# Kernel tuning notes

Measured on AMD Instinct MI355X. Metric: run time of the kernel, lower is better.

The kernel has to match this reference:

```python
import jax, jax.numpy as jnp
import numpy as np

N, IN_DIM, E, H, L, M = 65536, 512, 128, 4, 2, 256
DH = E // H  # 32

def _gaussian_orthogonal(m, d, rng):
    # FAVOR+ gaussian orthogonal random matrix (performer_pytorch, scaling=0)
    blocks = []
    for _ in range((m + d - 1) // d):
        q, _ = np.linalg.qr(rng.normal(size=(d, d)))
        blocks.append(q.T)
    mat = np.concatenate(blocks)[:m]
    mult = np.linalg.norm(rng.normal(size=(m, d)), axis=1)
    return (mult[:, None] * mat).astype(np.float32)

def setup_inputs() -> dict:
    rng = np.random.default_rng(0)
    r = lambda *s: jnp.asarray(rng.normal(size=s, scale=0.02), jnp.float32)
    z = lambda *s: jnp.zeros(s, jnp.float32)
    o = lambda *s: jnp.ones(s, jnp.float32)
    return dict(
        x=jnp.asarray(rng.normal(size=(N, IN_DIM)), dtype=jnp.float32),
        Wpin=r(IN_DIM, E), bpin=z(E),
        lag=o(L, E), lab=z(L, E),                    # performer inner pre-LN (attn)
        Wq=r(L, E, E), Wk=r(L, E, E), Wv=r(L, E, E), # qkv (no bias in performer_pytorch)
        Wo=r(L, E, E), bo=z(L, E),                   # attn to_out
        lbg=o(L, E), lbb=z(L, E),                    # performer inner pre-LN (ff)
        Wf1=r(L, E, 4 * E), bf1=z(L, 4 * E),         # performer inner GELU FFN
        Wf2=r(L, 4 * E, E), bf2=z(L, E),
        Wpo=r(L, E, E), bpo=z(L, E),                 # PerformerSelfAttention.out_proj
        n1g=o(L, E), n1b=z(L, E),                    # block norm1
        Wn1=r(L, E, 4 * E), bn1=z(L, 4 * E),         # block ReLU FFN
        Wn2=r(L, 4 * E, E), bn2=z(L, E),
        n2g=o(L, E), n2b=z(L, E),                    # block norm2
        Wc=r(E, 1), bc=z(1),                         # classifier
        proj=jnp.stack([jnp.asarray(_gaussian_orthogonal(M, DH, rng)) for _ in range(L)]),
    )

def _ln(x, g, b, eps=1e-5):
    mu = x.mean(-1, keepdims=True)
    var = ((x - mu) ** 2).mean(-1, keepdims=True)
    return (x - mu) * jax.lax.rsqrt(var + eps) * g + b

def _softmax_kernel(data, proj, is_query, eps=1e-4):
    # data: [1,H,N,DH]; proj: [M,DH]  (performer_pytorch softmax_kernel)
    dn = data.shape[-1] ** -0.25
    ratio = proj.shape[0] ** -0.5
    dd = jnp.einsum('bhnd,md->bhnm', data * dn, proj)
    diag = (data ** 2).sum(-1, keepdims=True) * 0.5 * (dn * dn)
    stab = jnp.max(dd, -1, keepdims=True) if is_query else jnp.max(dd)
    return ratio * (jnp.exp(dd - diag - stab) + eps)

def _linear_attn(qf, kf, v):
    # non-causal FAVOR+: O(N*M*DH)
    D = jnp.einsum('bhnm,bhm->bhn', qf, kf.sum(-2))          # denominator
    ctx = jnp.einsum('bhnm,bhnd->bhmd', kf, v)               # [1,H,M,DH]
    return jnp.einsum('bhnm,bhmd->bhnd', qf, ctx) / D[..., None]

def _forward(x, Wpin, bpin, lag, lab, Wq, Wk, Wv, Wo, bo, lbg, lbb,
             Wf1, bf1, Wf2, bf2, Wpo, bpo, n1g, n1b, Wn1, bn1, Wn2, bn2,
             n2g, n2b, Wc, bc, proj):
    h = (x @ Wpin + bpin)[None]  # [1,N,E]
    split = lambda t: t.reshape(1, -1, H, DH).transpose(0, 2, 1, 3)
    for l in range(L):
        # --- inner Performer (depth=1): pre-LN attn + pre-LN GELU FFN, residuals ---
        y = _ln(h, lag[l], lab[l])
        q, k, v = split(y @ Wq[l]), split(y @ Wk[l]), split(y @ Wv[l])
        qf = _softmax_kernel(q, proj[l], True)
        kf = _softmax_kernel(k, proj[l], False)
        a = _linear_attn(qf, kf, v).transpose(0, 2, 1, 3).reshape(1, -1, E)
        h1 = h + (a @ Wo[l] + bo[l])
        y2 = _ln(h1, lbg[l], lbb[l])
        h2 = h1 + (jax.nn.gelu(y2 @ Wf1[l] + bf1[l], approximate=False) @ Wf2[l] + bf2[l])
        # --- outer block: post-LN residual attn + post-LN ReLU FFN ---
        attn_out = h2 @ Wpo[l] + bpo[l]
        h = _ln(h + attn_out, n1g[l], n1b[l])
        ffn = jax.nn.relu(h @ Wn1[l] + bn1[l]) @ Wn2[l] + bn2[l]
        h = _ln(h + ffn, n2g[l], n2b[l])
    return jax.nn.sigmoid(h[0] @ Wc + bc)[:, 0]  # [N]

def reference(x, Wpin, bpin, lag, lab, Wq, Wk, Wv, Wo, bo, lbg, lbb,
              Wf1, bf1, Wf2, bf2, Wpo, bpo, n1g, n1b, Wn1, bn1, Wn2, bn2,
              n2g, n2b, Wc, bc, proj):
    return _forward(x, Wpin, bpin, lag, lab, Wq, Wk, Wv, Wo, bo, lbg, lbb,
                    Wf1, bf1, Wf2, bf2, Wpo, bpo, n1g, n1b, Wn1, bn1, Wn2, bn2,
                    n2g, n2b, Wc, bc, proj)
```

## Files before the change

### kernel.cpp

```cpp
#include <hip/hip_runtime.h>
#include <math.h>

#define NTOK  65536
#define EDIM  128
#define HN    4
#define DHD   32
#define MF    256
#define LLAYERS 2
#define INDIM 512
#define FDIM  512
#define CR    512
#define NCHK  (NTOK/CR)

#define DN    0.4204482076268573f
#define DN2   0.17677669529663687f
#define KEPS  1e-4f

typedef unsigned short u16;
typedef unsigned int   u32;
typedef __attribute__((ext_vector_type(8))) __bf16 bf16x8;
typedef __attribute__((ext_vector_type(4))) float  f32x4;

__device__ __forceinline__ u16 f2bf(float f){
  u32 u = __float_as_uint(f);
  u32 r = (u + 0x7fffu + ((u >> 16) & 1u)) >> 16;
  return (u16)r;
}
__device__ __forceinline__ float bf2f(u16 h){ return __uint_as_float(((u32)h) << 16); }

__device__ __forceinline__ void gload_lds16(const void* g, void* l){
  __builtin_amdgcn_global_load_lds(
      (const __attribute__((address_space(1))) u32*)g,
      (__attribute__((address_space(3))) u32*)l, 16, 0, 0);
}

struct PrepArgs {
  const float* Wpin; const float* Wq; const float* Wk; const float* Wv;
  const float* Wo;   const float* Wpo; const float* Wf1; const float* Wf2;
  const float* Wn1;  const float* Wn2; const float* proj;
};

__global__ __launch_bounds__(256) void prep_kernel(PrepArgs a, u16* __restrict__ wts,
                                                   u16* __restrict__ pjb)
{
  int idx = blockIdx.x * 256 + threadIdx.x;
  const float* sp; u16* dp; int r, K, J;
  if      (idx <  65536) { sp = a.Wpin; dp = wts;          r = idx;          K = 512; J = 128; }
  else if (idx <  98304) { sp = a.Wq;   dp = wts +  65536; r = idx -  65536; K = 128; J = 128; }
  else if (idx < 131072) { sp = a.Wk;   dp = wts +  98304; r = idx -  98304; K = 128; J = 128; }
  else if (idx < 163840) { sp = a.Wv;   dp = wts + 131072; r = idx - 131072; K = 128; J = 128; }
  else if (idx < 196608) { sp = a.Wo;   dp = wts + 163840; r = idx - 163840; K = 128; J = 128; }
  else if (idx < 229376) { sp = a.Wpo;  dp = wts + 196608; r = idx - 196608; K = 128; J = 128; }
  else if (idx < 360448) { sp = a.Wf1;  dp = wts + 229376; r = idx - 229376; K = 128; J = 512; }
  else if (idx < 491520) { sp = a.Wf2;  dp = wts + 360448; r = idx - 360448; K = 512; J = 128; }
  else if (idx < 622592) { sp = a.Wn1;  dp = wts + 491520; r = idx - 491520; K = 128; J = 512; }
  else if (idx < 753664) { sp = a.Wn2;  dp = wts + 622592; r = idx - 622592; K = 512; J = 128; }
  else { int p = idx - 753664; pjb[p] = f2bf(a.proj[p] * DN); return; }
  int kj = K * J;
  int l = r / kj, rr = r - l * kj;
  int j = rr / K, k = rr - j * K;
  dp[r] = f2bf(sp[(size_t)l * kj + (size_t)k * J + j]);
}

template<int LNM, bool A32, bool MULTI>
__global__ __launch_bounds__(256, 4) void gemm_f(
    const u16* __restrict__ A, const float* __restrict__ Af,
    const u16* __restrict__ Bt,
    const float* __restrict__ bias, const u16* __restrict__ res,
    u16* __restrict__ outRaw, int K, int J, int op,
    const float* __restrict__ g1, const float* __restrict__ b1, u16* __restrict__ outL1,
    u16* __restrict__ outAux,
    const float* __restrict__ Wcp, const float* __restrict__ bcp, float* __restrict__ outCls)
{
  __shared__ __align__(16) u16 pool[18432];
  __shared__ float lnred[2][2][32][2];
  u16* Al = pool;
  u16* Bl = pool + 6144;
  const int tid  = threadIdx.x;
  const int lane = tid & 63;
  const int w    = tid >> 6;
  const int wr   = w >> 1, wc = w & 1;
  const int bid  = blockIdx.x;
  const int nwg8 = gridDim.x >> 3;
  const int bsw  = (bid & 7) * nwg8 + (bid >> 3);
  const int n0   = bsw * 64;
  const int jb   = MULTI ? 0 : blockIdx.y * 128;
  const u16* Bu  = MULTI ? (Bt + (size_t)blockIdx.y * 32768) : Bt;

  f32x4 acc[2][4];
#pragma unroll
  for (int m = 0; m < 2; ++m)
#pragma unroll
    for (int n = 0; n < 4; ++n) acc[m][n] = (f32x4){0.f, 0.f, 0.f, 0.f};

  const int srow = lane >> 2;
  const int skg  = (lane & 3) ^ ((lane >> 3) & 3);

  auto stageB = [&](int buf, int k0) {
#pragma unroll
    for (int i = 0; i < 2; ++i) {
      const int rb = 2 * w + i;
      gload_lds16(Bu + (size_t)(jb + rb * 16 + srow) * K + k0 + skg * 8,
                  &Bl[buf * 4096 + rb * 512]);
    }
  };
  auto stageA16 = [&](int buf, int k0) {
    gload_lds16(A + (size_t)(n0 + w * 16 + srow) * K + k0 + skg * 8,
                &Al[buf * 2048 + w * 512]);
  };

  const int r16f = lane & 15;
  const int kgl  = (lane >> 4) ^ ((lane >> 1) & 3);
  const int foff = r16f * 32 + kgl * 8;

  auto compute = [&](int cur) {
    bf16x8 af[2], bfg[4];
#pragma unroll
    for (int m = 0; m < 2; ++m)
      af[m]  = *reinterpret_cast<const bf16x8*>(&Al[cur * 2048 + (wr * 2 + m) * 512 + foff]);
#pragma unroll
    for (int n = 0; n < 4; ++n)
      bfg[n] = *reinterpret_cast<const bf16x8*>(&Bl[cur * 4096 + (wc * 4 + n) * 512 + foff]);
#pragma unroll
    for (int m = 0; m < 2; ++m)
#pragma unroll
      for (int n = 0; n < 4; ++n)
        acc[m][n] = __builtin_amdgcn_mfma_f32_16x16x32_bf16(af[m], bfg[n], acc[m][n], 0, 0, 0);
  };

  if constexpr (A32) {
    constexpr int T = 16;
    float4 fA[3][2];
    const int r = tid >> 2, hf = tid & 3;
    auto loadA = [&](int slot, int k0) {
      const float* gp = Af + (size_t)(n0 + r) * 512 + k0 + hf * 8;
      fA[slot][0] = ((const float4*)gp)[0];
      fA[slot][1] = ((const float4*)gp)[1];
    };
    const int rbA = r >> 4, r16A = r & 15, swzA = (r16A >> 1) & 3;
    auto writeA = [&](int slot, int buf) {
      uint4 p0;
      p0.x = (u32)f2bf(fA[slot][0].x) | ((u32)f2bf(fA[slot][0].y) << 16);
      p0.y = (u32)f2bf(fA[slot][0].z) | ((u32)f2bf(fA[slot][0].w) << 16);
      p0.z = (u32)f2bf(fA[slot][1].x) | ((u32)f2bf(fA[slot][1].y) << 16);
      p0.w = (u32)f2bf(fA[slot][1].z) | ((u32)f2bf(fA[slot][1].w) << 16);
      *reinterpret_cast<uint4*>(&Al[buf * 2048 + rbA * 512 + r16A * 32 + (hf ^ swzA) * 8]) = p0;
    };
    loadA(0, 0); loadA(1, 32); loadA(2, 64);
    stageB(0, 0); stageB(1, 32);
    asm volatile("s_waitcnt vmcnt(8)" ::: "memory");
    writeA(0, 0);
#pragma unroll
    for (int t = 0; t < T; ++t) {
      if (t + 2 < T) asm volatile("s_waitcnt vmcnt(4) lgkmcnt(0)" ::: "memory");
      else           asm volatile("s_waitcnt vmcnt(0) lgkmcnt(0)" ::: "memory");
      __builtin_amdgcn_s_barrier();
      if (t + 1 < T) writeA((t + 1) % 3, (t + 1) % 3);
      if (t + 3 < T) loadA((t + 3) % 3, (t + 3) * 32);
      if (t + 2 < T) stageB((t + 2) % 3, (t + 2) * 32);
      compute(t % 3);
    }
    __builtin_amdgcn_s_barrier();
  } else {
    const int T = K >> 5;
    stageA16(0, 0); stageB(0, 0);
    stageA16(1, 32); stageB(1, 32);
    for (int t = 0; t < T; ++t) {
      if (t + 1 < T) asm volatile("s_waitcnt vmcnt(3) lgkmcnt(0)" ::: "memory");
      else           asm volatile("s_waitcnt vmcnt(0) lgkmcnt(0)" ::: "memory");
      __builtin_amdgcn_s_barrier();
      int cur = t % 3;
      if (t + 2 < T) { stageA16((t + 2) % 3, (t + 2) * 32); stageB((t + 2) % 3, (t + 2) * 32); }
      compute(cur);
    }
    __builtin_amdgcn_s_barrier();
  }

  const int colb = jb + wc * 64 + (lane & 15);
  const int rowb = n0 + wr * 32 + (lane >> 4) * 4;
  float bv[4];
#pragma unroll
  for (int n = 0; n < 4; ++n) bv[n] = bias ? bias[colb + n * 16] : 0.f;

  float v[2][4][4];
#pragma unroll
  for (int m = 0; m < 2; ++m)
#pragma unroll
    for (int n = 0; n < 4; ++n)
#pragma unroll
      for (int j = 0; j < 4; ++j) {
        float t = acc[m][n][j] + bv[n];
        if (res) t += bf2f(res[(size_t)(rowb + m * 16 + j) * J + colb + n * 16]);
        v[m][n][j] = t;
      }

  if constexpr (MULTI) {
    if (blockIdx.y == 2) {
      u16* tb = pool;
#pragma unroll
      for (int m = 0; m < 2; ++m)
#pragma unroll
        for (int n = 0; n < 4; ++n)
#pragma unroll
          for (int j = 0; j < 4; ++j)
            tb[(wc * 64 + n * 16 + (lane & 15)) * 72 + wr * 32 + m * 16 + (lane >> 4) * 4 + j]
                = f2bf(v[m][n][j]);
      __syncthreads();
      { const int c2 = tid >> 1, hf2 = tid & 1;
        const uint4* src = reinterpret_cast<const uint4*>(&tb[c2 * 72 + hf2 * 32]);
        uint4* dst = reinterpret_cast<uint4*>(outAux + (size_t)c2 * NTOK + n0 + hf2 * 32);
        dst[0] = src[0]; dst[1] = src[1]; dst[2] = src[2]; dst[3] = src[3]; }
      return;
    }
    u16* out0 = (blockIdx.y == 0) ? outRaw : outL1;
#pragma unroll
    for (int m = 0; m < 2; ++m)
#pragma unroll
      for (int n = 0; n < 4; ++n)
#pragma unroll
        for (int j = 0; j < 4; ++j)
          out0[(size_t)(rowb + m * 16 + j) * J + colb + n * 16] = f2bf(v[m][n][j]);
    return;
  }

  if (outRaw) {
#pragma unroll
    for (int m = 0; m < 2; ++m)
#pragma unroll
      for (int n = 0; n < 4; ++n)
#pragma unroll
        for (int j = 0; j < 4; ++j)
          outRaw[(size_t)(rowb + m * 16 + j) * J + colb + n * 16] = f2bf(v[m][n][j]);
  }

  if constexpr (LNM > 0 && !MULTI) {
    float rs[2][4], rq[2][4];
#pragma unroll
    for (int m = 0; m < 2; ++m)
#pragma unroll
      for (int j = 0; j < 4; ++j) {
        float s = 0.f, q = 0.f;
#pragma unroll
        for (int n = 0; n < 4; ++n) { float t = v[m][n][j]; s += t; q += t * t; }
        rs[m][j] = s; rq[m][j] = q;
      }
#pragma unroll
    for (int o = 1; o < 16; o <<= 1)
#pragma unroll
      for (int m = 0; m < 2; ++m)
#pragma unroll
        for (int j = 0; j < 4; ++j) {
          rs[m][j] += __shfl_xor(rs[m][j], o);
          rq[m][j] += __shfl_xor(rq[m][j], o);
        }
    __syncthreads();
    if ((lane & 15) == 0) {
#pragma unroll
      for (int m = 0; m < 2; ++m)
#pragma unroll
        for (int j = 0; j < 4; ++j) {
          int rloc = m * 16 + (lane >> 4) * 4 + j;
          lnred[wr][wc][rloc][0] = rs[m][j];
          lnred[wr][wc][rloc][1] = rq[m][j];
        }
    }
    __syncthreads();
    float gg[4], bb[4];
#pragma unroll
    for (int n = 0; n < 4; ++n) { gg[n] = g1[colb + n * 16]; bb[n] = b1[colb + n * 16]; }
#pragma unroll
    for (int m = 0; m < 2; ++m)
#pragma unroll
      for (int j = 0; j < 4; ++j) {
        int rloc = m * 16 + (lane >> 4) * 4 + j;
        float ts = rs[m][j] + lnred[wr][wc ^ 1][rloc][0];
        float tq = rq[m][j] + lnred[wr][wc ^ 1][rloc][1];
        float mu = ts * (1.f / 128.f);
        float rsig = rsqrtf(tq * (1.f / 128.f) - mu * mu + 1e-5f);
#pragma unroll
        for (int n = 0; n < 4; ++n)
          v[m][n][j] = (v[m][n][j] - mu) * rsig * gg[n] + bb[n];
      }
    if (outL1) {
#pragma unroll
      for (int m = 0; m < 2; ++m)
#pragma unroll
        for (int n = 0; n < 4; ++n)
#pragma unroll
          for (int j = 0; j < 4; ++j)
            outL1[(size_t)(rowb + m * 16 + j) * J + colb + n * 16] = f2bf(v[m][n][j]);
    }
  }
}

template<bool RESPOST, int ACT, int LNM>
__global__ __launch_bounds__(256, 2) void mega_f(
    const u16* __restrict__ A0, const u16* __restrict__ W0t,
    const float* __restrict__ b0p, const u16* __restrict__ res0,
    const float* __restrict__ g0, const float* __restrict__ bg0,
    const u16* __restrict__ W1t, const float* __restrict__ fb1p,
    const u16* __restrict__ W2t, const float* __restrict__ fb2p,
    u16* __restrict__ out,
    const float* __restrict__ g1, const float* __restrict__ bt1,
    u16* __restrict__ outL2, const float* __restrict__ g2, const float* __restrict__ bt2,
    const float* __restrict__ Wcp, const float* __restrict__ bcp, float* __restrict__ outCls)
{
  __shared__ __align__(16) u16 As[4][2048];
  __shared__ __align__(16) u16 Hs[4][2048];
  __shared__ __align__(16) u16 Bs[3][4096];
  __shared__ float lnred[2][2][32][2];
  const int tid  = threadIdx.x;
  const int lane = tid & 63;
  const int w    = tid >> 6;
  const int wr   = w >> 1, wc = w & 1;
  const int bid  = blockIdx.x;
  const int bsw  = (bid & 7) * (gridDim.x >> 3) + (bid >> 3);
  const int n0   = bsw * 64;

  const int srow = lane >> 2;
  const int skg  = (lane & 3) ^ ((lane >> 3) & 3);
  const int r16f = lane & 15;
  const int kgl  = (lane >> 4) ^ ((lane >> 1) & 3);
  const int foff = r16f * 32 + kgl * 8;
  const int colb = wc * 64 + (lane & 15);
  const int rowb = n0 + wr * 32 + (lane >> 4) * 4;

#pragma unroll
  for (int rb = 0; rb < 4; ++rb)
    gload_lds16(A0 + (size_t)(n0 + rb * 16 + srow) * EDIM + w * 32 + skg * 8, &As[w][rb * 512]);

  auto stageB = [&](int buf, int st) {
    const u16* base; size_t rstride; int kb0;
    if (st < 4) { base = W0t; rstride = 128; kb0 = st * 32; }
    else {
      int s2 = st - 4;
      int c = s2 >> 3, p = (s2 >> 2) & 1, kt = s2 & 3;
      if (p == 0) { base = W1t + (size_t)c * 16384; rstride = 128; kb0 = kt * 32; }
      else        { base = W2t;                      rstride = 512; kb0 = c * 128 + kt * 32; }
    }
#pragma unroll
    for (int i = 0; i < 2; ++i) {
      const int rb = 2 * w + i;
      gload_lds16(base + (size_t)(rb * 16 + srow) * rstride + kb0 + skg * 8, &Bs[buf][rb * 512]);
    }
  };

  stageB(0, 0);
  stageB(1, 1);

  f32x4 acc0[2][4], acc1[2][4], acc2[2][4];
#pragma unroll
  for (int m = 0; m < 2; ++m)
#pragma unroll
    for (int n = 0; n < 4; ++n) { acc0[m][n] = (f32x4){0.f,0.f,0.f,0.f}; acc2[m][n] = (f32x4){0.f,0.f,0.f,0.f}; }

  float v0[2][4][4];

#pragma unroll
  for (int st = 0; st < 36; ++st) {
    if (st + 1 < 36) asm volatile("s_waitcnt vmcnt(2) lgkmcnt(0)" ::: "memory");
    else             asm volatile("s_waitcnt vmcnt(0) lgkmcnt(0)" ::: "memory");
    __builtin_amdgcn_s_barrier();
    if (st + 2 < 36) stageB((st + 2) % 3, st + 2);

    if (st < 4) {
      const u16* Bc = &Bs[st % 3][0];
      bf16x8 af[2], bfg[4];
#pragma unroll
      for (int m = 0; m < 2; ++m) af[m]  = *reinterpret_cast<const bf16x8*>(&As[st][(wr * 2 + m) * 512 + foff]);
#pragma unroll
      for (int n = 0; n < 4; ++n) bfg[n] = *reinterpret_cast<const bf16x8*>(&Bc[(wc * 4 + n) * 512 + foff]);
#pragma unroll
      for (int m = 0; m < 2; ++m)
#pragma unroll
        for (int n = 0; n < 4; ++n)
          acc0[m][n] = __builtin_amdgcn_mfma_f32_16x16x32_bf16(af[m], bfg[n], acc0[m][n], 0, 0, 0);
      if (st == 3) {
        float bv0[4];
#pragma unroll
        for (int n = 0; n < 4; ++n) bv0[n] = b0p[colb + n * 16];
#pragma unroll
        for (int m = 0; m < 2; ++m)
#pragma unroll
          for (int n = 0; n < 4; ++n)
#pragma unroll
            for (int j = 0; j < 4; ++j)
              v0[m][n][j] = acc0[m][n][j] + bv0[n]
                  + bf2f(res0[(size_t)(rowb + m * 16 + j) * EDIM + colb + n * 16]);
        float rs[2][4], rq[2][4];
#pragma unroll
        for (int m = 0; m < 2; ++m)
#pragma unroll
          for (int j = 0; j < 4; ++j) {
            float s = 0.f, q = 0.f;
#pragma unroll
            for (int n = 0; n < 4; ++n) { float t = v0[m][n][j]; s += t; q += t * t; }
            rs[m][j] = s; rq[m][j] = q;
          }
#pragma unroll
        for (int o = 1; o < 16; o <<= 1)
#pragma unroll
          for (int m = 0; m < 2; ++m)
#pragma unroll
            for (int j = 0; j < 4; ++j) {
              rs[m][j] += __shfl_xor(rs[m][j], o);
              rq[m][j] += __shfl_xor(rq[m][j], o);
            }
        __syncthreads();
        if ((lane & 15) == 0) {
#pragma unroll
          for (int m = 0; m < 2; ++m)
#pragma unroll
            for (int j = 0; j < 4; ++j) {
              int rloc = m * 16 + (lane >> 4) * 4 + j;
              lnred[wr][wc][rloc][0] = rs[m][j];
              lnred[wr][wc][rloc][1] = rq[m][j];
            }
        }
        __syncthreads();
        float gg[4], bb[4];
#pragma unroll
        for (int n = 0; n < 4; ++n) { gg[n] = g0[colb + n * 16]; bb[n] = bg0[colb + n * 16]; }
#pragma unroll
        for (int m = 0; m < 2; ++m)
#pragma unroll
          for (int j = 0; j < 4; ++j) {
            int rloc = m * 16 + (lane >> 4) * 4 + j;
            float ts = rs[m][j] + lnred[wr][wc ^ 1][rloc][0];
            float tq = rq[m][j] + lnred[wr][wc ^ 1][rloc][1];
            float mu = ts * (1.f / 128.f);
            float rsig = rsqrtf(tq * (1.f / 128.f) - mu * mu + 1e-5f);
            const int r16 = (lane >> 4) * 4 + j;
            const int rb  = wr * 2 + m;
#pragma unroll
            for (int n = 0; n < 4; ++n) {
              float lnv = (v0[m][n][j] - mu) * rsig * gg[n] + bb[n];
              const int q = wc * 64 + n * 16 + (lane & 15);
              const int ts2 = q >> 5, ql = q & 31;
              const int s = (ql >> 3) ^ ((r16 >> 1) & 3);
              As[ts2][rb * 512 + r16 * 32 + s * 8 + (ql & 7)] = f2bf(lnv);
              if (RESPOST) v0[m][n][j] = lnv;
            }
          }
      }
    } else {
      const int s2 = st - 4;
      const int c = s2 >> 3, p = (s2 >> 2) & 1, kt = s2 & 3;
      if ((s2 & 7) == 0) {
#pragma unroll
        for (int m = 0; m < 2; ++m)
#pragma unroll
          for (int n = 0; n < 4; ++n) acc1[m][n] = (f32x4){0.f, 0.f, 0.f, 0.f};
      }
      const u16* Asrc = p ? &Hs[kt][0] : &As[kt][0];
      const u16* Bc = &Bs[st % 3][0];
      bf16x8 af[2], bfg[4];
#pragma unroll
      for (int m = 0; m < 2; ++m) af[m]  = *reinterpret_cast<const bf16x8*>(&Asrc[(wr * 2 + m) * 512 + foff]);
#pragma unroll
      for (int n = 0; n < 4; ++n) bfg[n] = *reinterpret_cast<const bf16x8*>(&Bc[(wc * 4 + n) * 512 + foff]);
      if (p == 0) {
#pragma unroll
        for (int m = 0; m < 2; ++m)
#pragma unroll
          for (int n = 0; n < 4; ++n)
            acc1[m][n] = __builtin_amdgcn_mfma_f32_16x16x32_bf16(af[m], bfg[n], acc1[m][n], 0, 0, 0);
      } else {
#pragma unroll
        for (int m = 0; m < 2; ++m)
#pragma unroll
          for (int n = 0; n < 4; ++n)
            acc2[m][n] = __builtin_amdgcn_mfma_f32_16x16x32_bf16(af[m], bfg[n], acc2[m][n], 0, 0, 0);
      }
      if ((s2 & 7) == 3) {
        float fb[4];
#pragma unroll
        for (int n = 0; n < 4; ++n) fb[n] = fb1p[c * 128 + wc * 64 + n * 16 + (lane & 15)];
#pragma unroll
        for (int m = 0; m < 2; ++m)
#pragma unroll
          for (int n = 0; n < 4; ++n)
#pragma unroll
            for (int j = 0; j < 4; ++j) {
              float t = acc1[m][n][j] + fb[n];
              if (ACT == 1) t = 0.5f * t * (1.f + erff(t * 0.70710678118654752f));
              else          t = fmaxf(t, 0.f);
              const int r16 = (lane >> 4) * 4 + j;
              const int rb  = wr * 2 + m;
              const int q   = wc * 64 + n * 16 + (lane & 15);
              const int ts2 = q >> 5, ql = q & 31;
              const int s   = (ql >> 3) ^ ((r16 >> 1) & 3);
              Hs[ts2][rb * 512 + r16 * 32 + s * 8 + (ql & 7)] = f2bf(t);
            }
      }
    }
  }

  float fb[4];
#pragma unroll
  for (int n = 0; n < 4; ++n) fb[n] = fb2p[colb + n * 16];
  float v[2][4][4];
#pragma unroll
  for (int m = 0; m < 2; ++m)
#pragma unroll
    for (int n = 0; n < 4; ++n)
#pragma unroll
      for (int j = 0; j < 4; ++j)
        v[m][n][j] = acc2[m][n][j] + fb[n] + v0[m][n][j];

  auto ln_apply = [&](const float* gp, const float* bp) {
    float rs[2][4], rq[2][4];
#pragma unroll
    for (int m = 0; m < 2; ++m)
#pragma unroll
      for (int j = 0; j < 4; ++j) {
        float s = 0.f, q = 0.f;
#pragma unroll
        for (int n = 0; n < 4; ++n) { float t = v[m][n][j]; s += t; q += t * t; }
        rs[m][j] = s; rq[m][j] = q;
      }
#pragma unroll
    for (int o = 1; o < 16; o <<= 1)
#pragma unroll
      for (int m = 0; m < 2; ++m)
#pragma unroll
        for (int j = 0; j < 4; ++j) {
          rs[m][j] += __shfl_xor(rs[m][j], o);
          rq[m][j] += __shfl_xor(rq[m][j], o);
        }
    __syncthreads();
    if ((lane & 15) == 0) {
#pragma unroll
      for (int m = 0; m < 2; ++m)
#pragma unroll
        for (int j = 0; j < 4; ++j) {
          int rloc = m * 16 + (lane >> 4) * 4 + j;
          lnred[wr][wc][rloc][0] = rs[m][j];
          lnred[wr][wc][rloc][1] = rq[m][j];
        }
    }
    __syncthreads();
    float gg[4], bb[4];
#pragma unroll
    for (int n = 0; n < 4; ++n) { gg[n] = gp[colb + n * 16]; bb[n] = bp[colb + n * 16]; }
#pragma unroll
    for (int m = 0; m < 2; ++m)
#pragma unroll
      for (int j = 0; j < 4; ++j) {
        int rloc = m * 16 + (lane >> 4) * 4 + j;
        float ts = rs[m][j] + lnred[wr][wc ^ 1][rloc][0];
        float tq = rq[m][j] + lnred[wr][wc ^ 1][rloc][1];
        float mu = ts * (1.f / 128.f);
        float rsig = rsqrtf(tq * (1.f / 128.f) - mu * mu + 1e-5f);
#pragma unroll
        for (int n = 0; n < 4; ++n)
          v[m][n][j] = (v[m][n][j] - mu) * rsig * gg[n] + bb[n];
      }
  };

  if constexpr (LNM > 0) ln_apply(g1, bt1);
#pragma unroll
  for (int m = 0; m < 2; ++m)
#pragma unroll
    for (int n = 0; n < 4; ++n)
#pragma unroll
      for (int j = 0; j < 4; ++j)
        out[(size_t)(rowb + m * 16 + j) * EDIM + colb + n * 16] = f2bf(v[m][n][j]);

  if constexpr (LNM == 2) {
    ln_apply(g2, bt2);
#pragma unroll
    for (int m = 0; m < 2; ++m)
#pragma unroll
      for (int n = 0; n < 4; ++n)
#pragma unroll
        for (int j = 0; j < 4; ++j)
          outL2[(size_t)(rowb + m * 16 + j) * EDIM + colb + n * 16] = f2bf(v[m][n][j]);
  }
  if constexpr (LNM == 3) {
    const float bc0 = bcp[0];
    float wv[4];
#pragma unroll
    for (int n = 0; n < 4; ++n) wv[n] = Wcp[colb + n * 16];
    float dp[2][4];
#pragma unroll
    for (int m = 0; m < 2; ++m)
#pragma unroll
      for (int j = 0; j < 4; ++j) {
        float s = 0.f;
#pragma unroll
        for (int n = 0; n < 4; ++n) s += v[m][n][j] * wv[n];
        dp[m][j] = s;
      }
#pragma unroll
    for (int o = 1; o < 16; o <<= 1)
#pragma unroll
      for (int m = 0; m < 2; ++m)
#pragma unroll
        for (int j = 0; j < 4; ++j) dp[m][j] += __shfl_xor(dp[m][j], o);
    __syncthreads();
    if ((lane & 15) == 0) {
#pragma unroll
      for (int m = 0; m < 2; ++m)
#pragma unroll
        for (int j = 0; j < 4; ++j)
          lnred[wr][wc][m * 16 + (lane >> 4) * 4 + j][0] = dp[m][j];
    }
    __syncthreads();
// ... 209 lines not shown
#pragma unroll
  for (int jf = 0; jf < 16; ++jf) {
    bf16x8 b = *reinterpret_cast<const bf16x8*>(pjb + (jf * 16 + c) * DHD + g * 8);
#pragma unroll
    for (int rf = 0; rf < 2; ++rf) {
      f32x4 d = __builtin_amdgcn_mfma_f32_16x16x32_bf16(af[rf], b, z, 0, 0, 0);
#pragma unroll
      for (int r = 0; r < 4; ++r) rmax[rf][r] = fmaxf(rmax[rf][r], d[r]);
    }
  }
#pragma unroll
  for (int rf = 0; rf < 2; ++rf)
#pragma unroll
    for (int r = 0; r < 4; ++r) {
      float vv = rmax[rf][r];
      vv = fmaxf(vv, __shfl_xor(vv, 1)); vv = fmaxf(vv, __shfl_xor(vv, 2));
      vv = fmaxf(vv, __shfl_xor(vv, 4)); vv = fmaxf(vv, __shfl_xor(vv, 8));
      rmax[rf][r] = vv;
    }
  float crow[2][4];
#pragma unroll
  for (int rf = 0; rf < 2; ++rf)
#pragma unroll
    for (int r = 0; r < 4; ++r)
      crow[rf][r] = 0.5f * DN2 * __shfl(s2[rf], (lane & 48) | (4 * g + r)) + rmax[rf][r];

  f32x4 oacc[2][2];
#pragma unroll
  for (int rf = 0; rf < 2; ++rf)
#pragma unroll
    for (int df = 0; df < 2; ++df) oacc[rf][df] = z;
  float Dacc[2][4];
#pragma unroll
  for (int rf = 0; rf < 2; ++rf)
#pragma unroll
    for (int r = 0; r < 4; ++r) Dacc[rf][r] = 0.f;

  for (int ks = 0; ks < 8; ++ks) {
#pragma unroll
    for (int jj = 0; jj < 2; ++jj) {
      const int jf = ks * 2 + jj;
      bf16x8 b = *reinterpret_cast<const bf16x8*>(pjb + (jf * 16 + c) * DHD + g * 8);
      const float ksv = ksg[h * MF + jf * 16 + c];
#pragma unroll
      for (int rf = 0; rf < 2; ++rf) {
        f32x4 d = __builtin_amdgcn_mfma_f32_16x16x32_bf16(af[rf], b, z, 0, 0, 0);
#pragma unroll
        for (int r = 0; r < 4; ++r) {
          float q = __expf(d[r] - crow[rf][r]) + KEPS;
          u16 qb_ = f2bf(q);
          qfs[w][(rf * 16 + 4 * g + r) * 40 + jj * 16 + c] = qb_;
          Dacc[rf][r] += bf2f(qb_) * ksv;
        }
      }
    }
#pragma unroll
    for (int rf = 0; rf < 2; ++rf) {
      bf16x8 a = *reinterpret_cast<const bf16x8*>(&qfs[w][(rf * 16 + c) * 40 + g * 8]);
#pragma unroll
      for (int df = 0; df < 2; ++df) {
        bf16x8 bc = *reinterpret_cast<const bf16x8*>(
            ctxT + (size_t)(h * DHD + df * 16 + c) * MF + ks * 32 + g * 8);
        oacc[rf][df] = __builtin_amdgcn_mfma_f32_16x16x32_bf16(a, bc, oacc[rf][df], 0, 0, 0);
      }
    }
  }
#pragma unroll
  for (int rf = 0; rf < 2; ++rf)
#pragma unroll
    for (int r = 0; r < 4; ++r) {
      float vv = Dacc[rf][r];
      vv += __shfl_xor(vv, 1); vv += __shfl_xor(vv, 2);
      vv += __shfl_xor(vv, 4); vv += __shfl_xor(vv, 8);
      Dacc[rf][r] = vv;
    }
#pragma unroll
  for (int rf = 0; rf < 2; ++rf)
#pragma unroll
    for (int df = 0; df < 2; ++df)
#pragma unroll
      for (int r = 0; r < 4; ++r)
        Am[(size_t)(n0 + rf * 16 + 4 * g + r) * EDIM + h * DHD + df * 16 + c] =
            f2bf(oacc[rf][df][r] / Dacc[rf][r]);
}

extern "C" void kernel_launch(void* const* d_in, const int* in_sizes, int n_in,
                              void* d_out, int out_size, void* d_ws, size_t ws_size,
                              hipStream_t stream)
{
  const float* x    = (const float*)d_in[0];
  const float* Wpin = (const float*)d_in[1];
  const float* bpin = (const float*)d_in[2];
  const float* lag  = (const float*)d_in[3];
  const float* lab  = (const float*)d_in[4];
  const float* Wq   = (const float*)d_in[5];
  const float* Wk   = (const float*)d_in[6];
  const float* Wv   = (const float*)d_in[7];
  const float* Wo   = (const float*)d_in[8];
  const float* bo   = (const float*)d_in[9];
  const float* lbg  = (const float*)d_in[10];
  const float* lbb  = (const float*)d_in[11];
  const float* Wf1  = (const float*)d_in[12];
  const float* bf1  = (const float*)d_in[13];
  const float* Wf2  = (const float*)d_in[14];
  const float* bf2  = (const float*)d_in[15];
  const float* Wpo  = (const float*)d_in[16];
  const float* bpo  = (const float*)d_in[17];
  const float* n1g  = (const float*)d_in[18];
  const float* n1b  = (const float*)d_in[19];
  const float* Wn1  = (const float*)d_in[20];
  const float* bn1  = (const float*)d_in[21];
  const float* Wn2  = (const float*)d_in[22];
  const float* bn2  = (const float*)d_in[23];
  const float* n2g  = (const float*)d_in[24];
  const float* n2b  = (const float*)d_in[25];
  const float* Wc   = (const float*)d_in[26];
  const float* bc   = (const float*)d_in[27];
  const float* proj = (const float*)d_in[28];

  size_t off = 0;
  char* base = (char*)d_ws;
  auto alloc = [&](size_t bytes) -> void* {
    void* p = base + off;
    off += (bytes + 255) & ~(size_t)255;
    return p;
  };
  u16* hb  = (u16*)alloc((size_t)NTOK * EDIM * 2);
  u16* yb  = (u16*)alloc((size_t)NTOK * EDIM * 2);
  u16* qb  = (u16*)alloc((size_t)NTOK * EDIM * 2);
  u16* kb  = (u16*)alloc((size_t)NTOK * EDIM * 2);
  u16* vb  = (u16*)alloc((size_t)NTOK * EDIM * 2);
  u16* VT  = (u16*)alloc((size_t)HN * DHD * NTOK * 2);
  u16* pjb = (u16*)alloc((size_t)LLAYERS * MF * DHD * 2);
  u16* ctxT = (u16*)alloc((size_t)HN * DHD * MF * 2);
  float* ksg  = (float*)alloc((size_t)HN * MF * 4);
  float* pctx = (float*)alloc((size_t)HN * NCHK * MF * DHD * 4);
  float* pks  = (float*)alloc((size_t)HN * NCHK * MF * 4);
  float* pvs  = (float*)alloc((size_t)HN * NCHK * DHD * 4);
  float* pmax = (float*)alloc((size_t)HN * NCHK * 4);
  u16* wts = (u16*)alloc((size_t)753664 * 2);

  u16* Wpint = wts;
  auto Wqt  = [&](int l){ return wts +  65536 + (size_t)l * 16384; };
  auto Wot  = [&](int l){ return wts + 163840 + (size_t)l * 16384; };
  auto Wpot = [&](int l){ return wts + 196608 + (size_t)l * 16384; };
  auto Wf1t = [&](int l){ return wts + 229376 + (size_t)l * 65536; };
  auto Wf2t = [&](int l){ return wts + 360448 + (size_t)l * 65536; };
  auto Wn1t = [&](int l){ return wts + 491520 + (size_t)l * 65536; };
  auto Wn2t = [&](int l){ return wts + 622592 + (size_t)l * 65536; };

  PrepArgs pa{Wpin, Wq, Wk, Wv, Wo, Wpo, Wf1, Wf2, Wn1, Wn2, proj};
  prep_kernel<<<3008, 256, 0, stream>>>(pa, wts, pjb);

  gemm_f<1, true, false><<<dim3(NTOK / 64, 1), 256, 0, stream>>>(
      nullptr, x, Wpint, bpin, nullptr, hb, INDIM, EDIM, 0,
      lag, lab, yb, nullptr, nullptr, nullptr, nullptr);

  for (int l = 0; l < LLAYERS; ++l) {
    const u16* pjl = pjb + (size_t)l * MF * DHD;

    gemm_f<0, false, true><<<dim3(NTOK / 64, 3), 256, 0, stream>>>(
        yb, nullptr, Wqt(l), nullptr, nullptr, qb, EDIM, EDIM, 0,
        nullptr, nullptr, kb, VT, nullptr, nullptr, nullptr);

    ctxk_kernel<<<dim3(NCHK, HN), 256, 0, stream>>>(kb, VT, pjl, pctx, pks, pvs, pmax);
    reduce_all<<<132, 256, 0, stream>>>(pctx, pks, pvs, pmax, ctxT, ksg);
    qout_kernel<<<dim3(NTOK / 128, HN), 256, 0, stream>>>(qb, pjl, ctxT, ksg, yb);

    mega_f<false, 1, 0><<<NTOK / 64, 256, 0, stream>>>(
        yb, Wot(l), bo + l * EDIM, hb, lbg + l * EDIM, lbb + l * EDIM,
        Wf1t(l), bf1 + l * FDIM, Wf2t(l), bf2 + l * EDIM, vb,
        nullptr, nullptr, nullptr, nullptr, nullptr, nullptr, nullptr, nullptr);

    if (l < LLAYERS - 1) {
      mega_f<true, 2, 2><<<NTOK / 64, 256, 0, stream>>>(
          vb, Wpot(l), bpo + l * EDIM, hb, n1g + l * EDIM, n1b + l * EDIM,
          Wn1t(l), bn1 + l * FDIM, Wn2t(l), bn2 + l * EDIM, hb,
          n2g + l * EDIM, n2b + l * EDIM,
          yb, lag + (l + 1) * EDIM, lab + (l + 1) * EDIM,
          nullptr, nullptr, nullptr);
    } else {
      mega_f<true, 2, 3><<<NTOK / 64, 256, 0, stream>>>(
          vb, Wpot(l), bpo + l * EDIM, hb, n1g + l * EDIM, n1b + l * EDIM,
          Wn1t(l), bn1 + l * FDIM, Wn2t(l), bn2 + l * EDIM, hb,
          n2g + l * EDIM, n2b + l * EDIM,
          nullptr, nullptr, nullptr,
          Wc, bc, (float*)d_out);
    }
  }
}
```

Before: 471.4 us.

## Fuse QKV projections into one block per row tile and deepen weight prefetch

The generic gemm_f template is split into a specialised input-projection kernel and a new qkv_f kernel. qkv_f loads the 64-row activation tile into LDS once and reuses it for the Q, K and V weight passes, so the activation is not re-read by three separate grid-y blocks. The mega_f kernels and qkv_f now keep four B-tile buffers with three stages in flight instead of three buffers with two. This trades more LDS per block, which may reduce occupancy, for less repeated activation traffic and more latency hiding.

```diff
diff --git a/kernel.cpp b/kernel.cpp
--- a/kernel.cpp
+++ b/kernel.cpp
@@ -62,30 +62,22 @@
   dp[r] = f2bf(sp[(size_t)l * kj + (size_t)k * J + j]);
 }
 
-template<int LNM, bool A32, bool MULTI>
-__global__ __launch_bounds__(256, 4) void gemm_f(
-    const u16* __restrict__ A, const float* __restrict__ Af,
-    const u16* __restrict__ Bt,
-    const float* __restrict__ bias, const u16* __restrict__ res,
-    u16* __restrict__ outRaw, int K, int J, int op,
-    const float* __restrict__ g1, const float* __restrict__ b1, u16* __restrict__ outL1,
-    u16* __restrict__ outAux,
-    const float* __restrict__ Wcp, const float* __restrict__ bcp, float* __restrict__ outCls)
+__global__ __launch_bounds__(256, 4) void gemm_in(
+    const float* __restrict__ Af, const u16* __restrict__ Bt,
+    const float* __restrict__ bias,
+    u16* __restrict__ outRaw,
+    const float* __restrict__ g1, const float* __restrict__ b1, u16* __restrict__ outL1)
 {
-  __shared__ __align__(16) u16 pool[18432];
+  __shared__ __align__(16) u16 Al[3][2048];
+  __shared__ __align__(16) u16 Bl[3][4096];
   __shared__ float lnred[2][2][32][2];
-  u16* Al = pool;
-  u16* Bl = pool + 6144;
   const int tid  = threadIdx.x;
   const int lane = tid & 63;
   const int w    = tid >> 6;
   const int wr   = w >> 1, wc = w & 1;
   const int bid  = blockIdx.x;
-  const int nwg8 = gridDim.x >> 3;
-  const int bsw  = (bid & 7) * nwg8 + (bid >> 3);
+  const int bsw  = (bid & 7) * (gridDim.x >> 3) + (bid >> 3);
   const int n0   = bsw * 64;
-  const int jb   = MULTI ? 0 : blockIdx.y * 128;
-  const u16* Bu  = MULTI ? (Bt + (size_t)blockIdx.y * 32768) : Bt;
 
   f32x4 acc[2][4];
 #pragma unroll
@@ -100,197 +92,236 @@
 #pragma unroll
     for (int i = 0; i < 2; ++i) {
       const int rb = 2 * w + i;
-      gload_lds16(Bu + (size_t)(jb + rb * 16 + srow) * K + k0 + skg * 8,
-                  &Bl[buf * 4096 + rb * 512]);
-    }
-  };
-  auto stageA16 = [&](int buf, int k0) {
-    gload_lds16(A + (size_t)(n0 + w * 16 + srow) * K + k0 + skg * 8,
-                &Al[buf * 2048 + w * 512]);
+      gload_lds16(Bt + (size_t)(rb * 16 + srow) * 512 + k0 + skg * 8,
+                  &Bl[buf][rb * 512]);
+    }
   };
 
   const int r16f = lane & 15;
   const int kgl  = (lane >> 4) ^ ((lane >> 1) & 3);
   const int foff = r16f * 32 + kgl * 8;
 
-  auto compute = [&](int cur) {
+  constexpr int T = 16;
+  float4 fA[3][2];
+  const int r = tid >> 2, hf = tid & 3;
+  auto loadA = [&](int slot, int k0) {
+    const float* gp = Af + (size_t)(n0 + r) * 512 + k0 + hf * 8;
+    fA[slot][0] = ((const float4*)gp)[0];
+    fA[slot][1] = ((const float4*)gp)[1];
+  };
+  const int rbA = r >> 4, r16A = r & 15, swzA = (r16A >> 1) & 3;
+  auto writeA = [&](int slot, int buf) {
+    uint4 p0;
+    p0.x = (u32)f2bf(fA[slot][0].x) | ((u32)f2bf(fA[slot][0].y) << 16);
+    p0.y = (u32)f2bf(fA[slot][0].z) | ((u32)f2bf(fA[slot][0].w) << 16);
+    p0.z = (u32)f2bf(fA[slot][1].x) | ((u32)f2bf(fA[slot][1].y) << 16);
+    p0.w = (u32)f2bf(fA[slot][1].z) | ((u32)f2bf(fA[slot][1].w) << 16);
+    *reinterpret_cast<uint4*>(&Al[buf][rbA * 512 + r16A * 32 + (hf ^ swzA) * 8]) = p0;
+  };
+  loadA(0, 0); loadA(1, 32); loadA(2, 64);
+  stageB(0, 0); stageB(1, 32);
+  asm volatile("s_waitcnt vmcnt(8)" ::: "memory");
+  writeA(0, 0);
+#pragma unroll
+  for (int t = 0; t < T; ++t) {
+    if (t + 2 < T) asm volatile("s_waitcnt vmcnt(4) lgkmcnt(0)" ::: "memory");
+    else           asm volatile("s_waitcnt vmcnt(0) lgkmcnt(0)" ::: "memory");
+    __builtin_amdgcn_s_barrier();
+    if (t + 1 < T) writeA((t + 1) % 3, (t + 1) % 3);
+    if (t + 3 < T) loadA((t + 3) % 3, (t + 3) * 32);
+    if (t + 2 < T) stageB((t + 2) % 3, (t + 2) * 32);
+    {
+      const int cur = t % 3;
+      bf16x8 af[2], bfg[4];
+#pragma unroll
+      for (int m = 0; m < 2; ++m)
+        af[m]  = *reinterpret_cast<const bf16x8*>(&Al[cur][(wr * 2 + m) * 512 + foff]);
+#pragma unroll
+      for (int n = 0; n < 4; ++n)
+        bfg[n] = *reinterpret_cast<const bf16x8*>(&Bl[cur][(wc * 4 + n) * 512 + foff]);
+#pragma unroll
+      for (int m = 0; m < 2; ++m)
+#pragma unroll
+        for (int n = 0; n < 4; ++n)
+          acc[m][n] = __builtin_amdgcn_mfma_f32_16x16x32_bf16(af[m], bfg[n], acc[m][n], 0, 0, 0);
+    }
+  }
+  __builtin_amdgcn_s_barrier();
+
+  const int colb = wc * 64 + (lane & 15);
+  const int rowb = n0 + wr * 32 + (lane >> 4) * 4;
+  float bv[4];
+#pragma unroll
+  for (int n = 0; n < 4; ++n) bv[n] = bias[colb + n * 16];
+
+  float v[2][4][4];
+#pragma unroll
+  for (int m = 0; m < 2; ++m)
+#pragma unroll
+    for (int n = 0; n < 4; ++n)
+#pragma unroll
+      for (int j = 0; j < 4; ++j)
+        v[m][n][j] = acc[m][n][j] + bv[n];
+
+#pragma unroll
+  for (int m = 0; m < 2; ++m)
+#pragma unroll
+    for (int n = 0; n < 4; ++n)
+#pragma unroll
+      for (int j = 0; j < 4; ++j)
+        outRaw[(size_t)(rowb + m * 16 + j) * EDIM + colb + n * 16] = f2bf(v[m][n][j]);
+
+  float rs[2][4], rq[2][4];
+#pragma unroll
+  for (int m = 0; m < 2; ++m)
+#pragma unroll
+    for (int j = 0; j < 4; ++j) {
+      float s = 0.f, q = 0.f;
+#pragma unroll
+      for (int n = 0; n < 4; ++n) { float t = v[m][n][j]; s += t; q += t * t; }
+      rs[m][j] = s; rq[m][j] = q;
+    }
+#pragma unroll
+  for (int o = 1; o < 16; o <<= 1)
+#pragma unroll
+    for (int m = 0; m < 2; ++m)
+#pragma unroll
+      for (int j = 0; j < 4; ++j) {
+        rs[m][j] += __shfl_xor(rs[m][j], o);
+        rq[m][j] += __shfl_xor(rq[m][j], o);
+      }
+  __syncthreads();
+  if ((lane & 15) == 0) {
+#pragma unroll
+    for (int m = 0; m < 2; ++m)
+#pragma unroll
+      for (int j = 0; j < 4; ++j) {
+        int rloc = m * 16 + (lane >> 4) * 4 + j;
+        lnred[wr][wc][rloc][0] = rs[m][j];
+        lnred[wr][wc][rloc][1] = rq[m][j];
+      }
+  }
+  __syncthreads();
+  float gg[4], bb[4];
+#pragma unroll
+  for (int n = 0; n < 4; ++n) { gg[n] = g1[colb + n * 16]; bb[n] = b1[colb + n * 16]; }
+#pragma unroll
+  for (int m = 0; m < 2; ++m)
+#pragma unroll
+    for (int j = 0; j < 4; ++j) {
+      int rloc = m * 16 + (lane >> 4) * 4 + j;
+      float ts = rs[m][j] + lnred[wr][wc ^ 1][rloc][0];
+      float tq = rq[m][j] + lnred[wr][wc ^ 1][rloc][1];
+      float mu = ts * (1.f / 128.f);
+      float rsig = rsqrtf(tq * (1.f / 128.f) - mu * mu + 1e-5f);
+#pragma unroll
+      for (int n = 0; n < 4; ++n)
+        outL1[(size_t)(rowb + m * 16 + j) * EDIM + colb + n * 16] =
+            f2bf((v[m][n][j] - mu) * rsig * gg[n] + bb[n]);
+    }
+}
+
+__global__ __launch_bounds__(256, 3) void qkv_f(
+    const u16* __restrict__ A0, const u16* __restrict__ Wt,
+    u16* __restrict__ qout, u16* __restrict__ kout, u16* __restrict__ vtout)
+{
+  __shared__ __align__(16) u16 As[4][2048];
+  __shared__ __align__(16) u16 Bs[4][4096];
+  const int tid  = threadIdx.x;
+  const int lane = tid & 63;
+  const int w    = tid >> 6;
+  const int wr   = w >> 1, wc = w & 1;
+  const int bid  = blockIdx.x;
+  const int bsw  = (bid & 7) * (gridDim.x >> 3) + (bid >> 3);
+  const int n0   = bsw * 64;
+
+  const int srow = lane >> 2;
+  const int skg  = (lane & 3) ^ ((lane >> 3) & 3);
+  const int r16f = lane & 15;
+  const int kgl  = (lane >> 4) ^ ((lane >> 1) & 3);
+  const int foff = r16f * 32 + kgl * 8;
+  const int colb = wc * 64 + (lane & 15);
+  const int rowb = n0 + wr * 32 + (lane >> 4) * 4;
+
+#pragma unroll
+  for (int rb = 0; rb < 4; ++rb)
+    gload_lds16(A0 + (size_t)(n0 + rb * 16 + srow) * EDIM + w * 32 + skg * 8, &As[w][rb * 512]);
+
+  auto stageB = [&](int buf, int st) {
+    const u16* base = Wt + (size_t)(st >> 2) * 32768;
+    const int kb0 = (st & 3) * 32;
+#pragma unroll
+    for (int i = 0; i < 2; ++i) {
+      const int rb = 2 * w + i;
+      gload_lds16(base + (size_t)(rb * 16 + srow) * 128 + kb0 + skg * 8, &Bs[buf][rb * 512]);
+    }
+  };
+  stageB(0, 0); stageB(1, 1); stageB(2, 2);
+
+  f32x4 acc[2][4];
+  float v[2][4][4];
+
+#pragma unroll
+  for (int st = 0; st < 12; ++st) {
+    if (st < 10)       asm volatile("s_waitcnt vmcnt(4) lgkmcnt(0)" ::: "memory");
+    else if (st == 10) asm volatile("s_waitcnt vmcnt(2) lgkmcnt(0)" ::: "memory");
+    else               asm volatile("s_waitcnt vmcnt(0) lgkmcnt(0)" ::: "memory");
+    __builtin_amdgcn_s_barrier();
+    if (st + 3 < 12) stageB((st + 3) & 3, st + 3);
+    if ((st & 3) == 0) {
+#pragma unroll
+      for (int m = 0; m < 2; ++m)
+#pragma unroll
+        for (int n = 0; n < 4; ++n) acc[m][n] = (f32x4){0.f, 0.f, 0.f, 0.f};
+    }
+    const int kt = st & 3;
     bf16x8 af[2], bfg[4];
 #pragma unroll
     for (int m = 0; m < 2; ++m)
-      af[m]  = *reinterpret_cast<const bf16x8*>(&Al[cur * 2048 + (wr * 2 + m) * 512 + foff]);
+      af[m]  = *reinterpret_cast<const bf16x8*>(&As[kt][(wr * 2 + m) * 512 + foff]);
 #pragma unroll
     for (int n = 0; n < 4; ++n)
-      bfg[n] = *reinterpret_cast<const bf16x8*>(&Bl[cur * 4096 + (wc * 4 + n) * 512 + foff]);
+      bfg[n] = *reinterpret_cast<const bf16x8*>(&Bs[st & 3][(wc * 4 + n) * 512 + foff]);
 #pragma unroll
     for (int m = 0; m < 2; ++m)
 #pragma unroll
       for (int n = 0; n < 4; ++n)
         acc[m][n] = __builtin_amdgcn_mfma_f32_16x16x32_bf16(af[m], bfg[n], acc[m][n], 0, 0, 0);
-  };
-
-  if constexpr (A32) {
-    constexpr int T = 16;
-    float4 fA[3][2];
-    const int r = tid >> 2, hf = tid & 3;
-    auto loadA = [&](int slot, int k0) {
-      const float* gp = Af + (size_t)(n0 + r) * 512 + k0 + hf * 8;
-      fA[slot][0] = ((const float4*)gp)[0];
-      fA[slot][1] = ((const float4*)gp)[1];
-    };
-    const int rbA = r >> 4, r16A = r & 15, swzA = (r16A >> 1) & 3;
-    auto writeA = [&](int slot, int buf) {
-      uint4 p0;
-      p0.x = (u32)f2bf(fA[slot][0].x) | ((u32)f2bf(fA[slot][0].y) << 16);
-      p0.y = (u32)f2bf(fA[slot][0].z) | ((u32)f2bf(fA[slot][0].w) << 16);
-      p0.z = (u32)f2bf(fA[slot][1].x) | ((u32)f2bf(fA[slot][1].y) << 16);
-      p0.w = (u32)f2bf(fA[slot][1].z) | ((u32)f2bf(fA[slot][1].w) << 16);
-      *reinterpret_cast<uint4*>(&Al[buf * 2048 + rbA * 512 + r16A * 32 + (hf ^ swzA) * 8]) = p0;
-    };
-    loadA(0, 0); loadA(1, 32); loadA(2, 64);
-    stageB(0, 0); stageB(1, 32);
-    asm volatile("s_waitcnt vmcnt(8)" ::: "memory");
-    writeA(0, 0);
-#pragma unroll
-    for (int t = 0; t < T; ++t) {
-      if (t + 2 < T) asm volatile("s_waitcnt vmcnt(4) lgkmcnt(0)" ::: "memory");
-      else           asm volatile("s_waitcnt vmcnt(0) lgkmcnt(0)" ::: "memory");
-      __builtin_amdgcn_s_barrier();
-      if (t + 1 < T) writeA((t + 1) % 3, (t + 1) % 3);
-      if (t + 3 < T) loadA((t + 3) % 3, (t + 3) * 32);
-      if (t + 2 < T) stageB((t + 2) % 3, (t + 2) * 32);
-      compute(t % 3);
-    }
-    __builtin_amdgcn_s_barrier();
-  } else {
-    const int T = K >> 5;
-    stageA16(0, 0); stageB(0, 0);
-    stageA16(1, 32); stageB(1, 32);
-    for (int t = 0; t < T; ++t) {
-      if (t + 1 < T) asm volatile("s_waitcnt vmcnt(3) lgkmcnt(0)" ::: "memory");
-      else           asm volatile("s_waitcnt vmcnt(0) lgkmcnt(0)" ::: "memory");
-      __builtin_amdgcn_s_barrier();
-      int cur = t % 3;
-      if (t + 2 < T) { stageA16((t + 2) % 3, (t + 2) * 32); stageB((t + 2) % 3, (t + 2) * 32); }
-      compute(cur);
-    }
-    __builtin_amdgcn_s_barrier();
-  }
-
-  const int colb = jb + wc * 64 + (lane & 15);
-  const int rowb = n0 + wr * 32 + (lane >> 4) * 4;
-  float bv[4];
-#pragma unroll
-  for (int n = 0; n < 4; ++n) bv[n] = bias ? bias[colb + n * 16] : 0.f;
-
-  float v[2][4][4];
+    if (st == 3 || st == 7) {
+      u16* out = (st == 3) ? qout : kout;
+#pragma unroll
+      for (int m = 0; m < 2; ++m)
+#pragma unroll
+        for (int n = 0; n < 4; ++n)
+#pragma unroll
+          for (int j = 0; j < 4; ++j)
+            out[(size_t)(rowb + m * 16 + j) * EDIM + colb + n * 16] = f2bf(acc[m][n][j]);
+    }
+    if (st == 11) {
+#pragma unroll
+      for (int m = 0; m < 2; ++m)
+#pragma unroll
+        for (int n = 0; n < 4; ++n)
+#pragma unroll
+          for (int j = 0; j < 4; ++j) v[m][n][j] = acc[m][n][j];
+    }
+  }
+
+  __syncthreads();
+  u16* tb = &Bs[0][0];
 #pragma unroll
   for (int m = 0; m < 2; ++m)
 #pragma unroll
     for (int n = 0; n < 4; ++n)
 #pragma unroll
-      for (int j = 0; j < 4; ++j) {
-        float t = acc[m][n][j] + bv[n];
-        if (res) t += bf2f(res[(size_t)(rowb + m * 16 + j) * J + colb + n * 16]);
-        v[m][n][j] = t;
-      }
-
-  if constexpr (MULTI) {
-    if (blockIdx.y == 2) {
-      u16* tb = pool;
-#pragma unroll
-      for (int m = 0; m < 2; ++m)
-#pragma unroll
-        for (int n = 0; n < 4; ++n)
-#pragma unroll
-          for (int j = 0; j < 4; ++j)
-            tb[(wc * 64 + n * 16 + (lane & 15)) * 72 + wr * 32 + m * 16 + (lane >> 4) * 4 + j]
-                = f2bf(v[m][n][j]);
-      __syncthreads();
-      { const int c2 = tid >> 1, hf2 = tid & 1;
-        const uint4* src = reinterpret_cast<const uint4*>(&tb[c2 * 72 + hf2 * 32]);
-        uint4* dst = reinterpret_cast<uint4*>(outAux + (size_t)c2 * NTOK + n0 + hf2 * 32);
-        dst[0] = src[0]; dst[1] = src[1]; dst[2] = src[2]; dst[3] = src[3]; }
-      return;
-    }
-    u16* out0 = (blockIdx.y == 0) ? outRaw : outL1;
-#pragma unroll
-    for (int m = 0; m < 2; ++m)
-#pragma unroll
-      for (int n = 0; n < 4; ++n)
-#pragma unroll
-        for (int j = 0; j < 4; ++j)
-          out0[(size_t)(rowb + m * 16 + j) * J + colb + n * 16] = f2bf(v[m][n][j]);
-    return;
-  }
-
-  if (outRaw) {
-#pragma unroll
-    for (int m = 0; m < 2; ++m)
-#pragma unroll
-      for (int n = 0; n < 4; ++n)
-#pragma unroll
-        for (int j = 0; j < 4; ++j)
-          outRaw[(size_t)(rowb + m * 16 + j) * J + colb + n * 16] = f2bf(v[m][n][j]);
-  }
-
-  if constexpr (LNM > 0 && !MULTI) {
-    float rs[2][4], rq[2][4];
-#pragma unroll
-    for (int m = 0; m < 2; ++m)
-#pragma unroll
-      for (int j = 0; j < 4; ++j) {
-        float s = 0.f, q = 0.f;
-#pragma unroll
-        for (int n = 0; n < 4; ++n) { float t = v[m][n][j]; s += t; q += t * t; }
-        rs[m][j] = s; rq[m][j] = q;
-      }
-#pragma unroll
-    for (int o = 1; o < 16; o <<= 1)
-#pragma unroll
-      for (int m = 0; m < 2; ++m)
-#pragma unroll
-        for (int j = 0; j < 4; ++j) {
-          rs[m][j] += __shfl_xor(rs[m][j], o);
-          rq[m][j] += __shfl_xor(rq[m][j], o);
-        }
-    __syncthreads();
-    if ((lane & 15) == 0) {
-#pragma unroll
-      for (int m = 0; m < 2; ++m)
-#pragma unroll
-        for (int j = 0; j < 4; ++j) {
-          int rloc = m * 16 + (lane >> 4) * 4 + j;
-          lnred[wr][wc][rloc][0] = rs[m][j];
-          lnred[wr][wc][rloc][1] = rq[m][j];
-        }
-    }
-    __syncthreads();
-    float gg[4], bb[4];
-#pragma unroll
-    for (int n = 0; n < 4; ++n) { gg[n] = g1[colb + n * 16]; bb[n] = b1[colb + n * 16]; }
-#pragma unroll
-    for (int m = 0; m < 2; ++m)
-#pragma unroll
-      for (int j = 0; j < 4; ++j) {
-        int rloc = m * 16 + (lane >> 4) * 4 + j;
-        float ts = rs[m][j] + lnred[wr][wc ^ 1][rloc][0];
-        float tq = rq[m][j] + lnred[wr][wc ^ 1][rloc][1];
-        float mu = ts * (1.f / 128.f);
-        float rsig = rsqrtf(tq * (1.f / 128.f) - mu * mu + 1e-5f);
-#pragma unroll
-        for (int n = 0; n < 4; ++n)
-          v[m][n][j] = (v[m][n][j] - mu) * rsig * gg[n] + bb[n];
-      }
-    if (outL1) {
-#pragma unroll
-      for (int m = 0; m < 2; ++m)
-#pragma unroll
-        for (int n = 0; n < 4; ++n)
-#pragma unroll
-          for (int j = 0; j < 4; ++j)
-            outL1[(size_t)(rowb + m * 16 + j) * J + colb + n * 16] = f2bf(v[m][n][j]);
-    }
-  }
+      for (int j = 0; j < 4; ++j)
+        tb[(wc * 64 + n * 16 + (lane & 15)) * 72 + wr * 32 + m * 16 + (lane >> 4) * 4 + j]
+            = f2bf(v[m][n][j]);
+  __syncthreads();
+  { const int c2 = tid >> 1, hf2 = tid & 1;
+    const uint4* src = reinterpret_cast<const uint4*>(&tb[c2 * 72 + hf2 * 32]);
+    uint4* dst = reinterpret_cast<uint4*>(vtout + (size_t)c2 * NTOK + n0 + hf2 * 32);
+    dst[0] = src[0]; dst[1] = src[1]; dst[2] = src[2]; dst[3] = src[3]; }
 }
 
 template<bool RESPOST, int ACT, int LNM>
@@ -307,7 +338,7 @@
 {
   __shared__ __align__(16) u16 As[4][2048];
   __shared__ __align__(16) u16 Hs[4][2048];
-  __shared__ __align__(16) u16 Bs[3][4096];
+  __shared__ __align__(16) u16 Bs[4][4096];
   __shared__ float lnred[2][2][32][2];
   const int tid  = threadIdx.x;
   const int lane = tid & 63;
@@ -345,8 +376,7 @@
     }
   };
 
-  stageB(0, 0);
-  stageB(1, 1);
+  stageB(0, 0); stageB(1, 1); stageB(2, 2);
 
   f32x4 acc0[2][4], acc1[2][4], acc2[2][4];
 #pragma unroll
@@ -358,13 +388,14 @@
 
 #pragma unroll
   for (int st = 0; st < 36; ++st) {
-    if (st + 1 < 36) asm volatile("s_waitcnt vmcnt(2) lgkmcnt(0)" ::: "memory");
-    else             asm volatile("s_waitcnt vmcnt(0) lgkmcnt(0)" ::: "memory");
+    if (st < 34)       asm volatile("s_waitcnt vmcnt(4) lgkmcnt(0)" ::: "memory");
+    else if (st == 34) asm volatile("s_waitcnt vmcnt(2) lgkmcnt(0)" ::: "memory");
+    else               asm volatile("s_waitcnt vmcnt(0) lgkmcnt(0)" ::: "memory");
     __builtin_amdgcn_s_barrier();
-    if (st + 2 < 36) stageB((st + 2) % 3, st + 2);
+    if (st + 3 < 36) stageB((st + 3) & 3, st + 3);
 
     if (st < 4) {
-      const u16* Bc = &Bs[st % 3][0];
+      const u16* Bc = &Bs[st & 3][0];
       bf16x8 af[2], bfg[4];
 #pragma unroll
       for (int m = 0; m < 2; ++m) af[m]  = *reinterpret_cast<const bf16x8*>(&As[st][(wr * 2 + m) * 512 + foff]);
@@ -453,7 +484,7 @@
           for (int n = 0; n < 4; ++n) acc1[m][n] = (f32x4){0.f, 0.f, 0.f, 0.f};
       }
       const u16* Asrc = p ? &Hs[kt][0] : &As[kt][0];
-      const u16* Bc = &Bs[st % 3][0];
+      const u16* Bc = &Bs[st & 3][0];
       bf16x8 af[2], bfg[4];
 #pragma unroll
       for (int m = 0; m < 2; ++m) af[m]  = *reinterpret_cast<const bf16x8*>(&Asrc[(wr * 2 + m) * 512 + foff]);
@@ -969,16 +1000,12 @@
   PrepArgs pa{Wpin, Wq, Wk, Wv, Wo, Wpo, Wf1, Wf2, Wn1, Wn2, proj};
   prep_kernel<<<3008, 256, 0, stream>>>(pa, wts, pjb);
 
-  gemm_f<1, true, false><<<dim3(NTOK / 64, 1), 256, 0, stream>>>(
-      nullptr, x, Wpint, bpin, nullptr, hb, INDIM, EDIM, 0,
-      lag, lab, yb, nullptr, nullptr, nullptr, nullptr);
+  gemm_in<<<NTOK / 64, 256, 0, stream>>>(x, Wpint, bpin, hb, lag, lab, yb);
 
   for (int l = 0; l < LLAYERS; ++l) {
     const u16* pjl = pjb + (size_t)l * MF * DHD;
 
-    gemm_f<0, false, true><<<dim3(NTOK / 64, 3), 256, 0, stream>>>(
-        yb, nullptr, Wqt(l), nullptr, nullptr, qb, EDIM, EDIM, 0,
-        nullptr, nullptr, kb, VT, nullptr, nullptr, nullptr);
+    qkv_f<<<NTOK / 64, 256, 0, stream>>>(yb, Wqt(l), qb, kb, VT);
 
     ctxk_kernel<<<dim3(NCHK, HN), 256, 0, stream>>>(kb, VT, pjl, pctx, pks, pvs, pmax);
     reduce_all<<<132, 256, 0, stream>>>(pctx, pks, pvs, pmax, ctxT, ksg);
```

Measured after the change: 460.4 us. 2.3% less time.
